# Optimization experiments

Measured on AMD Instinct MI355X. Metric: run time of the kernel, lower is better.

The kernel has to match this reference:

```python
import jax, jax.numpy as jnp
import numpy as np

N_NODES = 100000
N_EDGES = 1200000
EMBED_DIM = 64
N_LAYERS = 3


def setup_inputs() -> dict:
    key = jax.random.key(0)
    k1, k2, k3, k4 = jax.random.split(key, 4)
    embeddings = jax.random.normal(k1, (N_NODES, EMBED_DIM), dtype=jnp.float32)
    edge_weight = jax.random.uniform(k2, (N_EDGES,), dtype=jnp.float32)
    edge_src = jax.random.randint(k3, (N_EDGES,), 0, N_NODES, dtype=jnp.int32)
    edge_dst = jax.random.randint(k4, (N_EDGES,), 0, N_NODES, dtype=jnp.int32)
    return {"embeddings": embeddings, "edge_weight": edge_weight,
            "edge_src": edge_src, "edge_dst": edge_dst}


def _spmm(edge_src, edge_dst, edge_weight, x):
    # (A @ x)[d] = sum_{e: dst(e)=d} w[e] * x[src(e)]  -- COO SpMM via gather + segment_sum
    msgs = edge_weight[:, None] * x[edge_src]  # [E, D]
    return jax.ops.segment_sum(msgs, edge_dst, num_segments=N_NODES)


def reference(embeddings, edge_weight, edge_src, edge_dst):
    all_embeddings = [embeddings]
    ego = embeddings
    for _ in range(N_LAYERS):
        ego = _spmm(edge_src, edge_dst, edge_weight, ego)
        all_embeddings.append(ego)
    # stack layer outputs: [n_layers+1, N, D]
    return jnp.stack(all_embeddings, axis=0)
```

## Files before the change

kernel.cpp:

```cpp
#include <hip/hip_runtime.h>


#define N_NODES 100000
#define DIM 64
#define SCAN_CHUNK 1024


__global__ void hist_kernel(const int* __restrict__ edst, int* __restrict__ deg, int E) {
    int e = blockIdx.x * blockDim.x + threadIdx.x;
    if (e < E) atomicAdd(&deg[edst[e]], 1);
}

__global__ void scan1_kernel(const int* __restrict__ deg, int* __restrict__ off,
                             int* __restrict__ bsum, int n) {
    __shared__ int sdata[256];
    int tid = threadIdx.x;
    int base = blockIdx.x * SCAN_CHUNK + tid * 4;
    int v[4];
    #pragma unroll
    for (int i = 0; i < 4; ++i) v[i] = (base + i < n) ? deg[base + i] : 0;
    int tsum = v[0] + v[1] + v[2] + v[3];
    sdata[tid] = tsum;
    __syncthreads();
    for (int d = 1; d < 256; d <<= 1) {
        int t = (tid >= d) ? sdata[tid - d] : 0;
        __syncthreads();
        sdata[tid] += t;
        __syncthreads();
    }
    int excl = sdata[tid] - tsum;
    if (tid == 255) bsum[blockIdx.x] = sdata[255];
    int run = excl;
    #pragma unroll
    for (int i = 0; i < 4; ++i) {
        if (base + i < n) off[base + i] = run;
        run += v[i];
    }
}

__global__ void scan2_kernel(int* __restrict__ bsum, int nb) {
    __shared__ int s[128];
    int tid = threadIdx.x;
    int v = (tid < nb) ? bsum[tid] : 0;
    s[tid] = v;
    __syncthreads();
    for (int d = 1; d < 128; d <<= 1) {
        int t = (tid >= d) ? s[tid - d] : 0;
        __syncthreads();
        s[tid] += t;
        __syncthreads();
    }
    if (tid < nb) bsum[tid] = s[tid] - v;
}

__global__ void scan3_kernel(int* __restrict__ off, const int* __restrict__ bsum, int n) {
    int i = blockIdx.x * blockDim.x + threadIdx.x;
    if (i < n) off[i] += bsum[i / SCAN_CHUNK];
}

__global__ void scatter_kernel(const int* __restrict__ esrc, const int* __restrict__ edst,
                               const float* __restrict__ ew, const int* __restrict__ off,
                               int* __restrict__ cur, int2* __restrict__ pairs, int E) {
    int e = blockIdx.x * blockDim.x + threadIdx.x;
    if (e >= E) return;
    int d = edst[e];
    int p = off[d] + atomicAdd(&cur[d], 1);
    int2 pr;
    pr.x = esrc[e];
    pr.y = __float_as_int(ew[e]);
    pairs[p] = pr;
}


__global__ void spmm_csr_kernel(const float* __restrict__ x,
                                const int2* __restrict__ pairs,
                                const int* __restrict__ off,
                                const int* __restrict__ deg,
                                float* __restrict__ y) {
    int gtid = blockIdx.x * blockDim.x + threadIdx.x;
    int node = gtid >> 6;
    int lane = threadIdx.x & 63;
    int q  = lane >> 4;
    int ql = lane & 15;
    if (node >= N_NODES) return;
    int s0 = off[node];
    int n  = deg[node];
    float4 acc = make_float4(0.f, 0.f, 0.f, 0.f);
    for (int k = q; k < n; k += 4) {
        int2 pr = pairs[s0 + k];
        float w = __int_as_float(pr.y);
        const float4* row = (const float4*)(x + (size_t)pr.x * DIM);
        float4 v = row[ql];
        acc.x += w * v.x;
        acc.y += w * v.y;
        acc.z += w * v.z;
        acc.w += w * v.w;
    }
    acc.x += __shfl_xor(acc.x, 16); acc.y += __shfl_xor(acc.y, 16);
    acc.z += __shfl_xor(acc.z, 16); acc.w += __shfl_xor(acc.w, 16);
    acc.x += __shfl_xor(acc.x, 32); acc.y += __shfl_xor(acc.y, 32);
    acc.z += __shfl_xor(acc.z, 32); acc.w += __shfl_xor(acc.w, 32);
    if (q == 0) {
        float4* yrow = (float4*)(y + (size_t)node * DIM);
        yrow[ql] = acc;
    }
}


__global__ void spmm_atomic_kernel(const float* __restrict__ x, const float* __restrict__ ew,
                                   const int* __restrict__ esrc, const int* __restrict__ edst,
                                   float* __restrict__ y, int n_edges) {
    long long tid = (long long)blockIdx.x * blockDim.x + threadIdx.x;
    int e = (int)(tid >> 6);
    int d = (int)(tid & 63);
    if (e >= n_edges) return;
    int s = esrc[e]; int t = edst[e]; float w = ew[e];
    atomicAdd(&y[(long long)t * DIM + d], w * x[(long long)s * DIM + d]);
}

extern "C" void kernel_launch(void* const* d_in, const int* in_sizes, int n_in,
                              void* d_out, int out_size, void* d_ws, size_t ws_size,
                              hipStream_t stream) {
    const float* emb  = (const float*)d_in[0];
    const float* ew   = (const float*)d_in[1];
    const int*   esrc = (const int*)d_in[2];
    const int*   edst = (const int*)d_in[3];
    float* out = (float*)d_out;

    const int E = in_sizes[1];
    const size_t layer_elems = (size_t)N_NODES * DIM;

    size_t need = (size_t)E * 8 + (size_t)3 * N_NODES * 4 + 512;
    hipMemcpyAsync(out, emb, layer_elems * sizeof(float), hipMemcpyDeviceToDevice, stream);

    if (ws_size >= need) {
        char* w = (char*)d_ws;
        int2* pairs = (int2*)w;
        int* deg  = (int*)(w + (size_t)E * 8);
        int* cur  = deg + N_NODES;
        int* off  = cur + N_NODES;
        int* bsum = off + N_NODES;

        hipMemsetAsync(deg, 0, (size_t)2 * N_NODES * 4, stream);

        const int eb = (E + 255) / 256;
        hist_kernel<<<eb, 256, 0, stream>>>(edst, deg, E);

        const int nscan = (N_NODES + SCAN_CHUNK - 1) / SCAN_CHUNK;
        scan1_kernel<<<nscan, 256, 0, stream>>>(deg, off, bsum, N_NODES);
        scan2_kernel<<<1, 128, 0, stream>>>(bsum, nscan);
        scan3_kernel<<<(N_NODES + 255) / 256, 256, 0, stream>>>(off, bsum, N_NODES);

        scatter_kernel<<<eb, 256, 0, stream>>>(esrc, edst, ew, off, cur, pairs, E);

        const int nb = (N_NODES + 3) / 4;
        for (int l = 1; l <= 3; ++l) {
            spmm_csr_kernel<<<nb, 256, 0, stream>>>(
                out + (size_t)(l - 1) * layer_elems, pairs, off, deg,
                out + (size_t)l * layer_elems);
        }
    } else {
        hipMemsetAsync(out + layer_elems, 0, 3 * layer_elems * sizeof(float), stream);
        const long long total_threads = (long long)E * 64;
        const int blocks = (int)((total_threads + 255) / 256);
        for (int l = 1; l <= 3; ++l) {
            spmm_atomic_kernel<<<blocks, 256, 0, stream>>>(
                out + (size_t)(l - 1) * layer_elems, ew, esrc, edst,
                out + (size_t)l * layer_elems, E);
        }
    }
}
```

Baseline: 399.0 us.

## Partition histogram and scatter atomics by destination range across blocks

Splits the histogram and CSR scatter kernels so each block handles one edge slice and only the destinations that fall in one of eight node ranges. The goal is to keep each block's atomics within a smaller, cache-resident part of the degree and cursor arrays, and to read edst with vectorized int4 loads. In exchange, every edge index is read eight times and most loaded edges are filtered out, and the launch grid is fixed at 1024 blocks.

```diff
diff --git a/kernel.cpp b/kernel.cpp
--- a/kernel.cpp
+++ b/kernel.cpp
@@ -5,10 +5,33 @@
 #define DIM 64
 #define SCAN_CHUNK 1024
 
-
-__global__ void hist_kernel(const int* __restrict__ edst, int* __restrict__ deg, int E) {
-    int e = blockIdx.x * blockDim.x + threadIdx.x;
-    if (e < E) atomicAdd(&deg[edst[e]], 1);
+#define NR 8
+#define RSIZE ((N_NODES + NR - 1) / NR)
+#define SLICES 128
+
+
+__global__ void hist_range_kernel(const int* __restrict__ edst, int* __restrict__ deg,
+                                  int E, int chunk) {
+    const int r = blockIdx.x & (NR - 1);
+    const int s = blockIdx.x / NR;
+    const int lo = r * RSIZE;
+    const int hi = lo + RSIZE;
+    const int e0 = s * chunk;
+    if (e0 >= E) return;
+    const int e1 = min(e0 + chunk, E);
+    const int nv = (e1 - e0) >> 2;
+    const int4* v4 = (const int4*)(edst + e0);
+    for (int i = threadIdx.x; i < nv; i += blockDim.x) {
+        int4 d = v4[i];
+        if (d.x >= lo && d.x < hi) atomicAdd(&deg[d.x], 1);
+        if (d.y >= lo && d.y < hi) atomicAdd(&deg[d.y], 1);
+        if (d.z >= lo && d.z < hi) atomicAdd(&deg[d.z], 1);
+        if (d.w >= lo && d.w < hi) atomicAdd(&deg[d.w], 1);
+    }
+    for (int e = e0 + (nv << 2) + threadIdx.x; e < e1; e += blockDim.x) {
+        int d = edst[e];
+        if (d >= lo && d < hi) atomicAdd(&deg[d], 1);
+    }
 }
 
 __global__ void scan1_kernel(const int* __restrict__ deg, int* __restrict__ off,
@@ -58,17 +81,45 @@
     if (i < n) off[i] += bsum[i / SCAN_CHUNK];
 }
 
-__global__ void scatter_kernel(const int* __restrict__ esrc, const int* __restrict__ edst,
-                               const float* __restrict__ ew, const int* __restrict__ off,
-                               int* __restrict__ cur, int2* __restrict__ pairs, int E) {
-    int e = blockIdx.x * blockDim.x + threadIdx.x;
-    if (e >= E) return;
-    int d = edst[e];
-    int p = off[d] + atomicAdd(&cur[d], 1);
-    int2 pr;
-    pr.x = esrc[e];
-    pr.y = __float_as_int(ew[e]);
-    pairs[p] = pr;
+__global__ void scatter_range_kernel(const int* __restrict__ esrc, const int* __restrict__ edst,
+                                     const float* __restrict__ ew, const int* __restrict__ off,
+                                     int* __restrict__ cur, int2* __restrict__ pairs,
+                                     int E, int chunk) {
+    const int r = blockIdx.x & (NR - 1);
+    const int s = blockIdx.x / NR;
+    const int lo = r * RSIZE;
+    const int hi = lo + RSIZE;
+    const int e0 = s * chunk;
+    if (e0 >= E) return;
+    const int e1 = min(e0 + chunk, E);
+    const int nv = (e1 - e0) >> 2;
+    const int4* v4 = (const int4*)(edst + e0);
+    for (int i = threadIdx.x; i < nv; i += blockDim.x) {
+        int4 d = v4[i];
+        int ebase = e0 + (i << 2);
+        #pragma unroll
+        for (int j = 0; j < 4; ++j) {
+            int dj = (j == 0) ? d.x : (j == 1) ? d.y : (j == 2) ? d.z : d.w;
+            if (dj >= lo && dj < hi) {
+                int e = ebase + j;
+                int p = off[dj] + atomicAdd(&cur[dj], 1);
+                int2 pr;
+                pr.x = esrc[e];
+                pr.y = __float_as_int(ew[e]);
+                pairs[p] = pr;
+            }
+        }
+    }
+    for (int e = e0 + (nv << 2) + threadIdx.x; e < e1; e += blockDim.x) {
+        int dj = edst[e];
+        if (dj >= lo && dj < hi) {
+            int p = off[dj] + atomicAdd(&cur[dj], 1);
+            int2 pr;
+            pr.x = esrc[e];
+            pr.y = __float_as_int(ew[e]);
+            pairs[p] = pr;
+        }
+    }
 }
 
 
@@ -143,15 +194,17 @@
 
         hipMemsetAsync(deg, 0, (size_t)2 * N_NODES * 4, stream);
 
-        const int eb = (E + 255) / 256;
-        hist_kernel<<<eb, 256, 0, stream>>>(edst, deg, E);
+        const int chunk = (((E + SLICES - 1) / SLICES) + 3) & ~3;
+        const int rblocks = NR * SLICES;
+
+        hist_range_kernel<<<rblocks, 256, 0, stream>>>(edst, deg, E, chunk);
 
         const int nscan = (N_NODES + SCAN_CHUNK - 1) / SCAN_CHUNK;
         scan1_kernel<<<nscan, 256, 0, stream>>>(deg, off, bsum, N_NODES);
         scan2_kernel<<<1, 128, 0, stream>>>(bsum, nscan);
         scan3_kernel<<<(N_NODES + 255) / 256, 256, 0, stream>>>(off, bsum, N_NODES);
 
-        scatter_kernel<<<eb, 256, 0, stream>>>(esrc, edst, ew, off, cur, pairs, E);
+        scatter_range_kernel<<<rblocks, 256, 0, stream>>>(esrc, edst, ew, off, cur, pairs, E, chunk);
 
         const int nb = (N_NODES + 3) / 4;
         for (int l = 1; l <= 3; ++l) {
```

After: 406.5 us. About the same (+1.9%).

## Build CSR via two-pass bucketed radix partition and widen SpMM per-lane loads

Applied to the files above, without the earlier changes.

Replaces the per-node histogram, three-kernel scan and random scatter with a two-level build. Edges are first bucketed into 64-node buckets, with the bucket scatter split into 8 destination ranges so writes stay local. A per-bucket pass then sorts each bucket in shared memory and writes deg/off. The SpMM kernel now processes 8 edges concurrently per wavefront, with each lane loading two float4s. This needs twice the edge workspace, and packing the local index into the high bits of src assumes node ids fit in 20 bits.

```diff
diff --git a/kernel.cpp b/kernel.cpp
--- a/kernel.cpp
+++ b/kernel.cpp
@@ -3,7 +3,172 @@
 
 #define N_NODES 100000
 #define DIM 64
+
+#define BSH 6
+#define NBK ((N_NODES + 63) >> 6)
+#define NR 8
+#define BPR ((NBK + NR - 1) / NR)
+#define RSIZE (BPR << BSH)
+#define SLICES 256
+
 #define SCAN_CHUNK 1024
+
+
+__global__ void bhist_kernel(const int* __restrict__ edst, int* __restrict__ bcnt, int E) {
+    int i = blockIdx.x * blockDim.x + threadIdx.x;
+    int nv = E >> 2;
+    if (i < nv) {
+        int4 d = ((const int4*)edst)[i];
+        atomicAdd(&bcnt[d.x >> BSH], 1);
+        atomicAdd(&bcnt[d.y >> BSH], 1);
+        atomicAdd(&bcnt[d.z >> BSH], 1);
+        atomicAdd(&bcnt[d.w >> BSH], 1);
+    }
+    if (i == 0) {
+        for (int e = nv << 2; e < E; ++e) atomicAdd(&bcnt[edst[e] >> BSH], 1);
+    }
+}
+
+__global__ void bscan_kernel(const int* __restrict__ bcnt, int* __restrict__ bbase,
+                             int* __restrict__ bcur, int nbk) {
+    __shared__ int s[1024];
+    int t = threadIdx.x;
+    int i0 = 2 * t, i1 = 2 * t + 1;
+    int v0 = (i0 < nbk) ? bcnt[i0] : 0;
+    int v1 = (i1 < nbk) ? bcnt[i1] : 0;
+    s[t] = v0 + v1;
+    __syncthreads();
+    for (int d = 1; d < 1024; d <<= 1) {
+        int tt = (t >= d) ? s[t - d] : 0;
+        __syncthreads();
+        s[t] += tt;
+        __syncthreads();
+    }
+    int excl = s[t] - (v0 + v1);
+    if (i0 < nbk) { bbase[i0] = excl;      bcur[i0] = excl; }
+    if (i1 < nbk) { bbase[i1] = excl + v0; bcur[i1] = excl + v0; }
+    if (t == 1023) bbase[nbk] = s[1023];
+}
+
+__global__ void pass1_kernel(const int* __restrict__ esrc, const int* __restrict__ edst,
+                             const float* __restrict__ ew, int* __restrict__ bcur,
+                             int2* __restrict__ tmp, int E, int chunk) {
+    const int r = blockIdx.x & (NR - 1);
+    const int s = blockIdx.x / NR;
+    const int lo = r * RSIZE;
+    const int hi = min(lo + RSIZE, N_NODES);
+    const int e0 = s * chunk;
+    if (e0 >= E) return;
+    const int e1 = min(e0 + chunk, E);
+    const int nv = (e1 - e0) >> 2;
+    const int4*   s4 = (const int4*)(esrc + e0);
+    const int4*   d4 = (const int4*)(edst + e0);
+    const float4* w4 = (const float4*)(ew + e0);
+    for (int i = threadIdx.x; i < nv; i += blockDim.x) {
+        int4 dd = d4[i]; int4 ss = s4[i]; float4 ww = w4[i];
+        #pragma unroll
+        for (int j = 0; j < 4; ++j) {
+            int d = (j == 0) ? dd.x : (j == 1) ? dd.y : (j == 2) ? dd.z : dd.w;
+            if (d >= lo && d < hi) {
+                int src = (j == 0) ? ss.x : (j == 1) ? ss.y : (j == 2) ? ss.z : ss.w;
+                float w = (j == 0) ? ww.x : (j == 1) ? ww.y : (j == 2) ? ww.z : ww.w;
+                int b = d >> BSH;
+                int p = atomicAdd(&bcur[b], 1);
+                int2 pr;
+                pr.x = src | ((d & 63) << 20);
+                pr.y = __float_as_int(w);
+                tmp[p] = pr;
+            }
+        }
+    }
+    for (int e = e0 + (nv << 2) + threadIdx.x; e < e1; e += blockDim.x) {
+        int d = edst[e];
+        if (d >= lo && d < hi) {
+            int b = d >> BSH;
+            int p = atomicAdd(&bcur[b], 1);
+            int2 pr;
+            pr.x = esrc[e] | ((d & 63) << 20);
+            pr.y = __float_as_int(ew[e]);
+            tmp[p] = pr;
+        }
+    }
+}
+
+__global__ void pass2_kernel(const int2* __restrict__ tmp, const int* __restrict__ bbase,
+                             int2* __restrict__ pairs, int* __restrict__ deg,
+                             int* __restrict__ off) {
+    __shared__ int lpos[64];
+    __shared__ int ldeg[64];
+    const int b = blockIdx.x;
+    const int base = bbase[b];
+    const int n = bbase[b + 1] - base;
+    if (threadIdx.x < 64) ldeg[threadIdx.x] = 0;
+    __syncthreads();
+    for (int i = threadIdx.x; i < n; i += blockDim.x) {
+        atomicAdd(&ldeg[tmp[base + i].x >> 20], 1);
+    }
+    __syncthreads();
+    if (threadIdx.x < 64) {
+        int v = ldeg[threadIdx.x];
+        int p = v;
+        #pragma unroll
+        for (int d = 1; d < 64; d <<= 1) {
+            int t = __shfl_up(p, d);
+            if (threadIdx.x >= d) p += t;
+        }
+        int excl = p - v;
+        lpos[threadIdx.x] = excl;
+        int node = (b << BSH) + threadIdx.x;
+        if (node < N_NODES) { deg[node] = v; off[node] = base + excl; }
+    }
+    __syncthreads();
+    for (int i = threadIdx.x; i < n; i += blockDim.x) {
+        int2 pr = tmp[base + i];
+        int dl = pr.x >> 20;
+        int p = base + atomicAdd(&lpos[dl], 1);
+        pr.x &= 0xFFFFF;
+        pairs[p] = pr;
+    }
+}
+
+
+__global__ void spmm_csr_kernel(const float* __restrict__ x,
+                                const int2* __restrict__ pairs,
+                                const int* __restrict__ off,
+                                const int* __restrict__ deg,
+                                float* __restrict__ y) {
+    int gtid = blockIdx.x * blockDim.x + threadIdx.x;
+    int node = gtid >> 6;
+    int lane = threadIdx.x & 63;
+    int o  = lane >> 3;
+    int ol = lane & 7;
+    if (node >= N_NODES) return;
+    int s0 = off[node];
+    int n  = deg[node];
+    float4 a0 = make_float4(0.f, 0.f, 0.f, 0.f);
+    float4 a1 = make_float4(0.f, 0.f, 0.f, 0.f);
+    for (int k = o; k < n; k += 8) {
+        int2 pr = pairs[s0 + k];
+        float w = __int_as_float(pr.y);
+        const float4* row = (const float4*)(x + (size_t)pr.x * DIM);
+        float4 v0 = row[ol];
+        float4 v1 = row[ol + 8];
+        a0.x += w * v0.x; a0.y += w * v0.y; a0.z += w * v0.z; a0.w += w * v0.w;
+        a1.x += w * v1.x; a1.y += w * v1.y; a1.z += w * v1.z; a1.w += w * v1.w;
+    }
+    #pragma unroll
+    for (int d = 8; d <= 32; d <<= 1) {
+        a0.x += __shfl_xor(a0.x, d); a0.y += __shfl_xor(a0.y, d);
+        a0.z += __shfl_xor(a0.z, d); a0.w += __shfl_xor(a0.w, d);
+        a1.x += __shfl_xor(a1.x, d); a1.y += __shfl_xor(a1.y, d);
+        a1.z += __shfl_xor(a1.z, d); a1.w += __shfl_xor(a1.w, d);
+    }
+    if (o == 0) {
+        float4* yrow = (float4*)(y + (size_t)node * DIM);
+        yrow[ol]     = a0;
+        yrow[ol + 8] = a1;
+    }
+}
 
 
 __global__ void hist_kernel(const int* __restrict__ edst, int* __restrict__ deg, int E) {
@@ -72,41 +237,6 @@
 }
 
 
-__global__ void spmm_csr_kernel(const float* __restrict__ x,
-                                const int2* __restrict__ pairs,
-                                const int* __restrict__ off,
-                                const int* __restrict__ deg,
-                                float* __restrict__ y) {
-    int gtid = blockIdx.x * blockDim.x + threadIdx.x;
-    int node = gtid >> 6;
-    int lane = threadIdx.x & 63;
-    int q  = lane >> 4;
-    int ql = lane & 15;
-    if (node >= N_NODES) return;
-    int s0 = off[node];
-    int n  = deg[node];
-    float4 acc = make_float4(0.f, 0.f, 0.f, 0.f);
-    for (int k = q; k < n; k += 4) {
-        int2 pr = pairs[s0 + k];
-        float w = __int_as_float(pr.y);
-        const float4* row = (const float4*)(x + (size_t)pr.x * DIM);
-        float4 v = row[ql];
-        acc.x += w * v.x;
-        acc.y += w * v.y;
-        acc.z += w * v.z;
-        acc.w += w * v.w;
-    }
-    acc.x += __shfl_xor(acc.x, 16); acc.y += __shfl_xor(acc.y, 16);
-    acc.z += __shfl_xor(acc.z, 16); acc.w += __shfl_xor(acc.w, 16);
-    acc.x += __shfl_xor(acc.x, 32); acc.y += __shfl_xor(acc.y, 32);
-    acc.z += __shfl_xor(acc.z, 32); acc.w += __shfl_xor(acc.w, 32);
-    if (q == 0) {
-        float4* yrow = (float4*)(y + (size_t)node * DIM);
-        yrow[ql] = acc;
-    }
-}
-
-
 __global__ void spmm_atomic_kernel(const float* __restrict__ x, const float* __restrict__ ew,
                                    const int* __restrict__ esrc, const int* __restrict__ edst,
                                    float* __restrict__ y, int n_edges) {
@@ -130,10 +260,38 @@
     const int E = in_sizes[1];
     const size_t layer_elems = (size_t)N_NODES * DIM;
 
-    size_t need = (size_t)E * 8 + (size_t)3 * N_NODES * 4 + 512;
     hipMemcpyAsync(out, emb, layer_elems * sizeof(float), hipMemcpyDeviceToDevice, stream);
 
-    if (ws_size >= need) {
+    const size_t need_new = (size_t)E * 16 + (size_t)N_NODES * 8 + (size_t)(3 * NBK + 1) * 4 + 1024;
+    const size_t need_old = (size_t)E * 8 + (size_t)3 * N_NODES * 4 + 512;
+
+    if (ws_size >= need_new) {
+        char* w = (char*)d_ws;
+        int2* pairs = (int2*)w;
+        int2* tmp   = (int2*)(w + (size_t)E * 8);
+        int*  deg   = (int*)(w + (size_t)E * 16);
+        int*  off   = deg + N_NODES;
+        int*  bcnt  = off + N_NODES;
+        int*  bbase = bcnt + NBK;
+        int*  bcur  = bbase + NBK + 1;
+
+        hipMemsetAsync(bcnt, 0, (size_t)NBK * 4, stream);
+
+        const int nv = E >> 2;
+        bhist_kernel<<<(nv + 255) / 256, 256, 0, stream>>>(edst, bcnt, E);
+        bscan_kernel<<<1, 1024, 0, stream>>>(bcnt, bbase, bcur, NBK);
+
+        const int chunk = (((E + SLICES - 1) / SLICES) + 3) & ~3;
+        pass1_kernel<<<NR * SLICES, 256, 0, stream>>>(esrc, edst, ew, bcur, tmp, E, chunk);
+        pass2_kernel<<<NBK, 256, 0, stream>>>(tmp, bbase, pairs, deg, off);
+
+        const int nb = (N_NODES + 3) / 4;
+        for (int l = 1; l <= 3; ++l) {
+            spmm_csr_kernel<<<nb, 256, 0, stream>>>(
+                out + (size_t)(l - 1) * layer_elems, pairs, off, deg,
+                out + (size_t)l * layer_elems);
+        }
+    } else if (ws_size >= need_old) {
         char* w = (char*)d_ws;
         int2* pairs = (int2*)w;
         int* deg  = (int*)(w + (size_t)E * 8);
```

After: 755.1 us. 1.89x slower.
